# Kernel tuning notes

Measured on AMD Instinct MI355X. Metric: run time of the kernel, lower is better.

Reference implementation:

```python
import jax, jax.numpy as jnp
import numpy as np

B, C, H, W = 2, 256, 32, 32
PK, CK = 256, 256


def setup_inputs() -> dict:
    key = jax.random.key(0)
    ks = jax.random.split(key, 9)
    s = 1.0 / np.sqrt(C)
    return {
        'x': jax.random.normal(ks[0], (B, C, H, W), jnp.float32),
        'primary_indices': jax.random.randint(ks[1], (B, PK), 0, B * H * W),
        'compare_indices': jax.random.randint(ks[2], (B, CK), 0, B * H * W),
        'pre_w': jax.random.uniform(ks[3], (3, C, C), jnp.float32, -s, s),
        'pre_b': jax.random.uniform(ks[4], (3, C), jnp.float32, -s, s),
        'post_w': jax.random.uniform(ks[5], (2, C, C), jnp.float32, -s, s),
        'post_b': jax.random.uniform(ks[6], (2, C), jnp.float32, -s, s),
        'post_out_w': jax.random.uniform(ks[7], (2, C), jnp.float32, -s, s),
        'post_out_b': jax.random.uniform(ks[8], (2,), jnp.float32, -s, s),
    }


def reference(x, primary_indices, compare_indices, pre_w, pre_b,
              post_w, post_b, post_out_w, post_out_b):
    # pre_compare: stack of 1x1 convs (c->c->c->c), ReLU between layers
    h = x
    for i in range(3):
        h = jnp.einsum('bchw,oc->bohw', h, pre_w[i]) + pre_b[i][None, :, None, None]
        if i < 2:
            h = jax.nn.relu(h)
    bs, c, hh, ww = h.shape
    # flatten to [bs*h*w, c] node features (matches torch transpose+reshape)
    flat = h.reshape(bs, c, hh * ww).transpose(0, 2, 1).reshape(bs * hh * ww, c)
    # gather primary / compare node features with global flat indices
    xp = flat[primary_indices.reshape(-1)].reshape(bs, -1, c).transpose(0, 2, 1)  # [b,c,pk]
    xc = flat[compare_indices.reshape(-1)].reshape(bs, -1, c).transpose(0, 2, 1)  # [b,c,ck]
    # broadcast pairwise squared difference -> [b,c,pk,ck]
    xx = (xp[:, :, :, None] - xc[:, :, None, :]) ** 2
    # post_compare: 1x1 conv stack c->c->c->2, ReLU between layers
    g = xx
    for i in range(2):
        g = jax.nn.relu(jnp.einsum('bcpq,oc->bopq', g, post_w[i]) + post_b[i][None, :, None, None])
    out = jnp.einsum('bcpq,oc->bopq', g, post_out_w) + post_out_b[None, :, None, None]
    return out  # [b, 2, pk, ck]
```

## Files before the change

### kernel.cpp

```cpp
#include <hip/hip_runtime.h>

typedef unsigned short u16;
typedef short bf16x8 __attribute__((ext_vector_type(8)));
typedef float f32x4 __attribute__((ext_vector_type(4)));
typedef u16 u16x4 __attribute__((ext_vector_type(4)));

__device__ __forceinline__ float b2f(u16 h) {
  unsigned u = ((unsigned)h) << 16;
  return __builtin_bit_cast(float, u);
}
__device__ __forceinline__ u16 f2b(float f) {
  unsigned u = __builtin_bit_cast(unsigned, f);
  u = u + 0x7fffu + ((u >> 16) & 1u);
  return (u16)(u >> 16);
}
__device__ __forceinline__ void gld_lds16(const void* g, void* l) {
  __builtin_amdgcn_global_load_lds(
      (__attribute__((address_space(1))) void*)(g),
      (__attribute__((address_space(3))) void*)(l), 16, 0, 0);
}

__global__ void dense_edge_prep(const float* __restrict__ x,
                                const float* __restrict__ pre_w,
                                const float* __restrict__ post_w,
                                u16* __restrict__ wb, u16* __restrict__ xt) {
  const int blk = blockIdx.x;
  const int t = threadIdx.x;
  if (blk < 160) {
    const int id = blk * 256 + t;
    const int layer = id >> 13;
    const int sid = id & 8191;
    const int m = sid >> 5;
    const int s8 = sid & 31;
    const float* src = (layer < 2) ? (post_w + layer * 65536)
                                   : (pre_w + (layer - 2) * 65536);
    u16* dst = wb + layer * 65536;
    f32x4 a = *(const f32x4*)(src + m * 256 + s8 * 8);
    f32x4 c = *(const f32x4*)(src + m * 256 + s8 * 8 + 4);
    bf16x8 o;
#pragma unroll
    for (int j = 0; j < 4; j++) o[j] = (short)f2b(a[j]);
#pragma unroll
    for (int j = 0; j < 4; j++) o[4 + j] = (short)f2b(c[j]);
    *(bf16x8*)(dst + (s8 * 256 + m) * 8) = o;
  } else {
    __shared__ float tile[32 * 65];
    const int xb = blk - 160;
    const int b = xb >> 7;
    const int ct = (xb >> 4) & 7;
    const int ht = xb & 15;
    const int c0 = ct * 32, hw0 = ht * 64;
#pragma unroll
    for (int rep = 0; rep < 8; rep++) {
      const int idx = rep * 256 + t;
      const int cl = idx >> 6, hl = idx & 63;
      tile[cl * 65 + hl] = x[(b * 256 + c0 + cl) * 1024 + hw0 + hl];
    }
    __syncthreads();
    const int hl = t >> 2, c8 = t & 3;
    bf16x8 o;
#pragma unroll
    for (int i = 0; i < 8; i++) o[i] = (short)f2b(tile[(c8 * 8 + i) * 65 + hl]);
    *(bf16x8*)(xt + (b * 1024 + hw0 + hl) * 256 + c0 + c8 * 8) = o;
  }
}

__global__ __launch_bounds__(256, 2) void dense_edge_pre(
    const u16* __restrict__ xt, const u16* __restrict__ wpre,
    const float* __restrict__ preb, u16* __restrict__ flat) {
  __shared__ u16 feat[2][4096];
  const int t = threadIdx.x;
  const int wv = t >> 6, ln = t & 63;
  const int nb = blockIdx.x * 16;
  const int q4 = ln >> 4, r15 = ln & 15;

#pragma unroll
  for (int i = 0; i < 2; i++) {
    const int slot = wv * 128 + i * 64 + ln;
    const int s8 = slot >> 4, nl = slot & 15;
    gld_lds16(xt + (nb + nl) * 256 + s8 * 8, &feat[0][slot * 8]);
  }
  __syncthreads();

#pragma unroll
  for (int l = 0; l < 3; l++) {
    const u16* wl = wpre + l * 65536;
    f32x4 acc[4];
    f32x4 zero = {0.f, 0.f, 0.f, 0.f};
#pragma unroll
    for (int mt = 0; mt < 4; mt++) acc[mt] = zero;
#pragma unroll
    for (int s = 0; s < 8; s++) {
      bf16x8 bv = *(const bf16x8*)(&feat[l & 1][((s * 4 + q4) * 16 + r15) * 8]);
#pragma unroll
      for (int mt = 0; mt < 4; mt++) {
        bf16x8 av = *(const bf16x8*)(wl + ((s * 4 + q4) * 256 + wv * 64 + mt * 16 + r15) * 8);
        acc[mt] = __builtin_amdgcn_mfma_f32_16x16x32_bf16(av, bv, acc[mt], 0, 0, 0);
      }
    }
    if (l < 2) {
#pragma unroll
      for (int mt = 0; mt < 4; mt++) {
        const int o = wv * 64 + mt * 16 + q4 * 4;
        f32x4 bb = *(const f32x4*)(preb + l * 256 + o);
        u16x4 pk;
#pragma unroll
        for (int r = 0; r < 4; r++) {
          float v = fmaxf(acc[mt][r] + bb[r], 0.f);
          pk[r] = f2b(v);
        }
        *(u16x4*)(&feat[(l + 1) & 1][((o >> 3) * 16 + r15) * 8 + (o & 7)]) = pk;
      }
      __syncthreads();
    } else {
#pragma unroll
      for (int mt = 0; mt < 4; mt++) {
        const int o = wv * 64 + mt * 16 + q4 * 4;
        f32x4 bb = *(const f32x4*)(preb + 512 + o);
        u16x4 pk;
#pragma unroll
        for (int r = 0; r < 4; r++) pk[r] = f2b(acc[mt][r] + bb[r]);
        *(u16x4*)(flat + (nb + r15) * 256 + o) = pk;
      }
    }
  }
}

__global__ __launch_bounds__(512, 2) void dense_edge_main(
    const u16* __restrict__ flat, const int* __restrict__ pidx,
    const int* __restrict__ cidx, const u16* __restrict__ w1s,
    const u16* __restrict__ w2s, const float* __restrict__ b1,
    const float* __restrict__ b2, const float* __restrict__ w3,
    const float* __restrict__ b3, float* __restrict__ out) {
  __shared__ u16 xxbuf[16384];
  __shared__ u16 t1buf[16384];
  __shared__ float pbuf[4][2][64];

  const int t = threadIdx.x;
  const int wv = t >> 6;
  const int ln = t & 63;
  const int q4 = ln >> 4, r15 = ln & 15;
  const bool prod = wv < 4;
  const int cw = wv & 3;
  const int blk = blockIdx.x;
  const int tile0 = blk * 8;
  const int b = tile0 >> 10;
  const int pt = (tile0 >> 5) & 31;
  const int qt0 = tile0 & 31;
  const int p0 = pt * 8;

  const u16* wsrc = prod ? w1s : w2s;
  bf16x8 af_w[4][8];
#pragma unroll
  for (int s = 0; s < 8; s++)
#pragma unroll
    for (int mt = 0; mt < 4; mt++)
      af_w[mt][s] = *(const bf16x8*)(wsrc + ((s * 4 + q4) * 256 + cw * 64 + mt * 16 + r15) * 8);

  int pn = 0;
  if (prod) pn = pidx[b * 256 + p0 + (ln >> 3)];
  const u16* prow = flat + pn * 256 + cw * 64;

#pragma unroll 1
  for (int j = 0; j <= 8; j++) {
    if (prod) {
      if (j < 8) {
        const int qn = cidx[b * 256 + (qt0 + j) * 8 + (ln & 7)];
        const u16* qrow = flat + qn * 256 + cw * 64;
#pragma unroll
        for (int i = 0; i < 8; i++) {
          bf16x8 av = *(const bf16x8*)(prow + i * 8);
          bf16x8 bv = *(const bf16x8*)(qrow + i * 8);
          bf16x8 ov;
#pragma unroll
          for (int jj = 0; jj < 8; jj++) {
            float d = b2f((u16)av[jj]) - b2f((u16)bv[jj]);
            ov[jj] = (short)f2b(d * d);
          }
          *(bf16x8*)(xxbuf + ((cw * 8 + i) * 64 + ln) * 8) = ov;
        }
      }
    } else if (j > 0) {
      f32x4 acc[4][4];
      {
        f32x4 zero = {0.f, 0.f, 0.f, 0.f};
#pragma unroll
        for (int mt = 0; mt < 4; mt++)
#pragma unroll
          for (int nt = 0; nt < 4; nt++) acc[mt][nt] = zero;
      }
#pragma unroll
      for (int s = 0; s < 8; s++) {
        bf16x8 bfr[4];
#pragma unroll
        for (int nt = 0; nt < 4; nt++)
          bfr[nt] = *(const bf16x8*)(t1buf + ((s * 4 + q4) * 64 + nt * 16 + r15) * 8);
#pragma unroll
        for (int mt = 0; mt < 4; mt++)
#pragma unroll
          for (int nt = 0; nt < 4; nt++)
            acc[mt][nt] = __builtin_amdgcn_mfma_f32_16x16x32_bf16(af_w[mt][s], bfr[nt], acc[mt][nt], 0, 0, 0);
      }
      float part[2][4] = {{0.f, 0.f, 0.f, 0.f}, {0.f, 0.f, 0.f, 0.f}};
#pragma unroll
      for (int mt = 0; mt < 4; mt++) {
        const int o = cw * 64 + mt * 16 + q4 * 4;
        f32x4 bb = *(const f32x4*)(b2 + o);
        f32x4 w3a = *(const f32x4*)(w3 + o);
        f32x4 w3b = *(const f32x4*)(w3 + 256 + o);
#pragma unroll
        for (int nt = 0; nt < 4; nt++) {
#pragma unroll
          for (int r = 0; r < 4; r++) {
            float v = fmaxf(acc[mt][nt][r] + bb[r], 0.f);
            part[0][nt] += v * w3a[r];
            part[1][nt] += v * w3b[r];
          }
        }
      }
#pragma unroll
      for (int o3 = 0; o3 < 2; o3++)
#pragma unroll
        for (int nt = 0; nt < 4; nt++) {
          part[o3][nt] += __shfl_xor(part[o3][nt], 16, 64);
          part[o3][nt] += __shfl_xor(part[o3][nt], 32, 64);
        }
      if (q4 == 0) {
#pragma unroll
        for (int o3 = 0; o3 < 2; o3++)
#pragma unroll
          for (int nt = 0; nt < 4; nt++)
            pbuf[cw][o3][nt * 16 + r15] = part[o3][nt];
      }
    }
    __syncthreads();

    if (prod) {
      if (j < 8) {
        f32x4 acc[4][4];
        {
          f32x4 zero = {0.f, 0.f, 0.f, 0.f};
#pragma unroll
          for (int mt = 0; mt < 4; mt++)
#pragma unroll
            for (int nt = 0; nt < 4; nt++) acc[mt][nt] = zero;
        }
#pragma unroll
        for (int s = 0; s < 8; s++) {
          bf16x8 bfr[4];
#pragma unroll
          for (int nt = 0; nt < 4; nt++)
            bfr[nt] = *(const bf16x8*)(xxbuf + ((s * 4 + q4) * 64 + nt * 16 + r15) * 8);
#pragma unroll
          for (int mt = 0; mt < 4; mt++)
#pragma unroll
            for (int nt = 0; nt < 4; nt++)
              acc[mt][nt] = __builtin_amdgcn_mfma_f32_16x16x32_bf16(af_w[mt][s], bfr[nt], acc[mt][nt], 0, 0, 0);
        }
#pragma unroll
        for (int mt = 0; mt < 4; mt++) {
          const int o = cw * 64 + mt * 16 + q4 * 4;
          f32x4 bb = *(const f32x4*)(b1 + o);
#pragma unroll
          for (int nt = 0; nt < 4; nt++) {
            const int nn = nt * 16 + r15;
            u16x4 pk;
#pragma unroll
            for (int r = 0; r < 4; r++) {
              float v = fmaxf(acc[mt][nt][r] + bb[r], 0.f);
              pk[r] = f2b(v);
            }
            *(u16x4*)(t1buf + ((o >> 3) * 64 + nn) * 8 + (o & 7)) = pk;
          }
        }
      }
    } else if (j > 0) {
      const int idx = t & 255;
      if (idx < 128) {
        const int o3 = idx >> 6;
        const int n = idx & 63;
        float v = pbuf[0][o3][n] + pbuf[1][o3][n] + pbuf[2][o3][n] + pbuf[3][o3][n] + b3[o3];
        out[((b * 2 + o3) * 256 + p0 + (n >> 3)) * 256 + (qt0 + j - 1) * 8 + (n & 7)] = v;
      }
    }
    __syncthreads();
  }
}

extern "C" void kernel_launch(void* const* d_in, const int* in_sizes, int n_in,
                              void* d_out, int out_size, void* d_ws, size_t ws_size,
                              hipStream_t stream) {
  (void)in_sizes; (void)n_in; (void)out_size; (void)ws_size;
  const float* x          = (const float*)d_in[0];
  const int*   pidx       = (const int*)d_in[1];
  const int*   cidx       = (const int*)d_in[2];
  const float* pre_w      = (const float*)d_in[3];
  const float* pre_b      = (const float*)d_in[4];
  const float* post_w     = (const float*)d_in[5];
  const float* post_b     = (const float*)d_in[6];
  const float* post_out_w = (const float*)d_in[7];
  const float* post_out_b = (const float*)d_in[8];
  float* out = (float*)d_out;

  u16* ws   = (u16*)d_ws;
  u16* wb   = ws;
  u16* w1s  = wb;
  u16* w2s  = wb + 65536;
  u16* wpre = wb + 131072;
  u16* xt   = ws + 327680;
  u16* flat = ws + 851968;

  dense_edge_prep<<<416, 256, 0, stream>>>(x, pre_w, post_w, wb, xt);
  dense_edge_pre<<<128, 256, 0, stream>>>(xt, wpre, pre_b, flat);
  dense_edge_main<<<256, 512, 0, stream>>>(flat, pidx, cidx, w1s, w2s,
                                           post_b, post_b + 256,
                                           post_out_w, post_out_b, out);
}
```

Baseline: 124.3 us.

## Fuse prep into pre-conv kernel, double main-kernel waves, use packed bf16 converts

Merges the weight/input prep kernel and the pre-compare conv kernel into one launch. The pre-conv weights are now read as fp32 from global memory and converted in-register rather than pre-converted, and the x transpose is done through LDS inside the conv kernel. The main kernel goes from 512 to 1024 threads, with 8 producer and 8 consumer waves each covering 32 output channels instead of 64, which lowers per-wave register use. bf16 rounding uses the packed hardware convert when it is available. This removes one launch and the xt round trip, at the cost of redundant fp32 weight loads and converts in every pre-conv block.

```diff
diff --git a/kernel.cpp b/kernel.cpp
--- a/kernel.cpp
+++ b/kernel.cpp
@@ -14,77 +14,91 @@
   u = u + 0x7fffu + ((u >> 16) & 1u);
   return (u16)(u >> 16);
 }
-__device__ __forceinline__ void gld_lds16(const void* g, void* l) {
-  __builtin_amdgcn_global_load_lds(
-      (__attribute__((address_space(1))) void*)(g),
-      (__attribute__((address_space(3))) void*)(l), 16, 0, 0);
-}
-
-__global__ void dense_edge_prep(const float* __restrict__ x,
-                                const float* __restrict__ pre_w,
-                                const float* __restrict__ post_w,
-                                u16* __restrict__ wb, u16* __restrict__ xt) {
+
+#if defined(__has_builtin)
+#if __has_builtin(__builtin_amdgcn_cvt_pk_bf16_f32)
+#define HAVE_CVT_PK_BF16 1
+#endif
+#endif
+
+__device__ __forceinline__ unsigned f2b_pk(float a, float b) {
+#ifdef HAVE_CVT_PK_BF16
+  auto v = __builtin_amdgcn_cvt_pk_bf16_f32(a, b);
+  unsigned r;
+  __builtin_memcpy(&r, &v, 4);
+  return r;
+#else
+  return (unsigned)f2b(a) | (((unsigned)f2b(b)) << 16);
+#endif
+}
+__device__ __forceinline__ bf16x8 pack8(const float* v) {
+  union { unsigned u[4]; bf16x8 o; } r;
+  r.u[0] = f2b_pk(v[0], v[1]);
+  r.u[1] = f2b_pk(v[2], v[3]);
+  r.u[2] = f2b_pk(v[4], v[5]);
+  r.u[3] = f2b_pk(v[6], v[7]);
+  return r.o;
+}
+__device__ __forceinline__ u16x4 pack4(float a, float b, float c, float d) {
+  union { unsigned u[2]; u16x4 o; } r;
+  r.u[0] = f2b_pk(a, b);
+  r.u[1] = f2b_pk(c, d);
+  return r.o;
+}
+
+__global__ __launch_bounds__(256, 2) void dense_edge_k1(
+    const float* __restrict__ x, const float* __restrict__ pre_w,
+    const float* __restrict__ preb, const float* __restrict__ post_w,
+    u16* __restrict__ wpost, u16* __restrict__ flat) {
   const int blk = blockIdx.x;
   const int t = threadIdx.x;
-  if (blk < 160) {
-    const int id = blk * 256 + t;
+  if (blk >= 128) {
+    const int id = (blk - 128) * 256 + t;
     const int layer = id >> 13;
     const int sid = id & 8191;
     const int m = sid >> 5;
     const int s8 = sid & 31;
-    const float* src = (layer < 2) ? (post_w + layer * 65536)
-                                   : (pre_w + (layer - 2) * 65536);
-    u16* dst = wb + layer * 65536;
-    f32x4 a = *(const f32x4*)(src + m * 256 + s8 * 8);
-    f32x4 c = *(const f32x4*)(src + m * 256 + s8 * 8 + 4);
-    bf16x8 o;
-#pragma unroll
-    for (int j = 0; j < 4; j++) o[j] = (short)f2b(a[j]);
-#pragma unroll
-    for (int j = 0; j < 4; j++) o[4 + j] = (short)f2b(c[j]);
-    *(bf16x8*)(dst + (s8 * 256 + m) * 8) = o;
-  } else {
-    __shared__ float tile[32 * 65];
-    const int xb = blk - 160;
-    const int b = xb >> 7;
-    const int ct = (xb >> 4) & 7;
-    const int ht = xb & 15;
-    const int c0 = ct * 32, hw0 = ht * 64;
-#pragma unroll
-    for (int rep = 0; rep < 8; rep++) {
-      const int idx = rep * 256 + t;
-      const int cl = idx >> 6, hl = idx & 63;
-      tile[cl * 65 + hl] = x[(b * 256 + c0 + cl) * 1024 + hw0 + hl];
-    }
-    __syncthreads();
-    const int hl = t >> 2, c8 = t & 3;
-    bf16x8 o;
-#pragma unroll
-    for (int i = 0; i < 8; i++) o[i] = (short)f2b(tile[(c8 * 8 + i) * 65 + hl]);
-    *(bf16x8*)(xt + (b * 1024 + hw0 + hl) * 256 + c0 + c8 * 8) = o;
-  }
-}
-
-__global__ __launch_bounds__(256, 2) void dense_edge_pre(
-    const u16* __restrict__ xt, const u16* __restrict__ wpre,
-    const float* __restrict__ preb, u16* __restrict__ flat) {
+    const float* src = post_w + layer * 65536 + m * 256 + s8 * 8;
+    f32x4 a = *(const f32x4*)(src);
+    f32x4 c = *(const f32x4*)(src + 4);
+    float tmp[8] = {a[0], a[1], a[2], a[3], c[0], c[1], c[2], c[3]};
+    *(bf16x8*)(wpost + layer * 65536 + (s8 * 256 + m) * 8) = pack8(tmp);
+    return;
+  }
+  __shared__ float xtile[256 * 20];
   __shared__ u16 feat[2][4096];
-  const int t = threadIdx.x;
   const int wv = t >> 6, ln = t & 63;
-  const int nb = blockIdx.x * 16;
   const int q4 = ln >> 4, r15 = ln & 15;
-
-#pragma unroll
-  for (int i = 0; i < 2; i++) {
-    const int slot = wv * 128 + i * 64 + ln;
-    const int s8 = slot >> 4, nl = slot & 15;
-    gld_lds16(xt + (nb + nl) * 256 + s8 * 8, &feat[0][slot * 8]);
+  const int nb = blk * 16;
+  const int b = nb >> 10;
+  const int hw0 = nb & 1023;
+
+  {
+    const float* src = x + (b * 256 + t) * 1024 + hw0;
+    f32x4 v0 = *(const f32x4*)(src);
+    f32x4 v1 = *(const f32x4*)(src + 4);
+    f32x4 v2 = *(const f32x4*)(src + 8);
+    f32x4 v3 = *(const f32x4*)(src + 12);
+    *(f32x4*)&xtile[t * 20 + 0] = v0;
+    *(f32x4*)&xtile[t * 20 + 4] = v1;
+    *(f32x4*)&xtile[t * 20 + 8] = v2;
+    *(f32x4*)&xtile[t * 20 + 12] = v3;
   }
   __syncthreads();
+#pragma unroll
+  for (int rep = 0; rep < 2; rep++) {
+    const int id = rep * 256 + t;
+    const int n = id & 15, s8 = id >> 4;
+    float tmp[8];
+#pragma unroll
+    for (int j = 0; j < 8; j++) tmp[j] = xtile[(s8 * 8 + j) * 20 + n];
+    *(bf16x8*)(&feat[0][(s8 * 16 + n) * 8]) = pack8(tmp);
+  }
+  __syncthreads();
 
 #pragma unroll
   for (int l = 0; l < 3; l++) {
-    const u16* wl = wpre + l * 65536;
+    const float* wl = pre_w + l * 65536;
     f32x4 acc[4];
     f32x4 zero = {0.f, 0.f, 0.f, 0.f};
 #pragma unroll
@@ -94,7 +108,11 @@
       bf16x8 bv = *(const bf16x8*)(&feat[l & 1][((s * 4 + q4) * 16 + r15) * 8]);
 #pragma unroll
       for (int mt = 0; mt < 4; mt++) {
-        bf16x8 av = *(const bf16x8*)(wl + ((s * 4 + q4) * 256 + wv * 64 + mt * 16 + r15) * 8);
+        const float* wp = wl + (wv * 64 + mt * 16 + r15) * 256 + (s * 4 + q4) * 8;
+        f32x4 wa = *(const f32x4*)(wp);
+        f32x4 wc = *(const f32x4*)(wp + 4);
+        float tmp[8] = {wa[0], wa[1], wa[2], wa[3], wc[0], wc[1], wc[2], wc[3]};
+        bf16x8 av = pack8(tmp);
         acc[mt] = __builtin_amdgcn_mfma_f32_16x16x32_bf16(av, bv, acc[mt], 0, 0, 0);
       }
     }
@@ -103,13 +121,12 @@
       for (int mt = 0; mt < 4; mt++) {
         const int o = wv * 64 + mt * 16 + q4 * 4;
         f32x4 bb = *(const f32x4*)(preb + l * 256 + o);
-        u16x4 pk;
-#pragma unroll
-        for (int r = 0; r < 4; r++) {
-          float v = fmaxf(acc[mt][r] + bb[r], 0.f);
-          pk[r] = f2b(v);
-        }
-        *(u16x4*)(&feat[(l + 1) & 1][((o >> 3) * 16 + r15) * 8 + (o & 7)]) = pk;
+        float v0 = fmaxf(acc[mt][0] + bb[0], 0.f);
+        float v1 = fmaxf(acc[mt][1] + bb[1], 0.f);
+        float v2 = fmaxf(acc[mt][2] + bb[2], 0.f);
+        float v3 = fmaxf(acc[mt][3] + bb[3], 0.f);
+        *(u16x4*)(&feat[(l + 1) & 1][((o >> 3) * 16 + r15) * 8 + (o & 7)]) =
+            pack4(v0, v1, v2, v3);
       }
       __syncthreads();
     } else {
@@ -117,16 +134,15 @@
       for (int mt = 0; mt < 4; mt++) {
         const int o = wv * 64 + mt * 16 + q4 * 4;
         f32x4 bb = *(const f32x4*)(preb + 512 + o);
-        u16x4 pk;
-#pragma unroll
-        for (int r = 0; r < 4; r++) pk[r] = f2b(acc[mt][r] + bb[r]);
-        *(u16x4*)(flat + (nb + r15) * 256 + o) = pk;
+        *(u16x4*)(flat + (nb + r15) * 256 + o) =
+            pack4(acc[mt][0] + bb[0], acc[mt][1] + bb[1],
+                  acc[mt][2] + bb[2], acc[mt][3] + bb[3]);
       }
     }
   }
 }
 
-__global__ __launch_bounds__(512, 2) void dense_edge_main(
+__global__ __launch_bounds__(1024, 4) void dense_edge_main(
     const u16* __restrict__ flat, const int* __restrict__ pidx,
     const int* __restrict__ cidx, const u16* __restrict__ w1s,
     const u16* __restrict__ w2s, const float* __restrict__ b1,
@@ -134,14 +150,14 @@
     const float* __restrict__ b3, float* __restrict__ out) {
   __shared__ u16 xxbuf[16384];
   __shared__ u16 t1buf[16384];
-  __shared__ float pbuf[4][2][64];
+  __shared__ float pbuf[8][2][64];
 
   const int t = threadIdx.x;
   const int wv = t >> 6;
   const int ln = t & 63;
   const int q4 = ln >> 4, r15 = ln & 15;
-  const bool prod = wv < 4;
-  const int cw = wv & 3;
+  const bool prod = wv < 8;
+  const int cw = wv & 7;
   const int blk = blockIdx.x;
   const int tile0 = blk * 8;
   const int b = tile0 >> 10;
@@ -150,42 +166,42 @@
   const int p0 = pt * 8;
 
   const u16* wsrc = prod ? w1s : w2s;
-  bf16x8 af_w[4][8];
+  bf16x8 af_w[2][8];
 #pragma unroll
   for (int s = 0; s < 8; s++)
 #pragma unroll
-    for (int mt = 0; mt < 4; mt++)
-      af_w[mt][s] = *(const bf16x8*)(wsrc + ((s * 4 + q4) * 256 + cw * 64 + mt * 16 + r15) * 8);
+    for (int mt = 0; mt < 2; mt++)
+      af_w[mt][s] = *(const bf16x8*)(wsrc + ((s * 4 + q4) * 256 + cw * 32 + mt * 16 + r15) * 8);
 
   int pn = 0;
   if (prod) pn = pidx[b * 256 + p0 + (ln >> 3)];
-  const u16* prow = flat + pn * 256 + cw * 64;
+  const u16* prow = flat + pn * 256 + cw * 32;
 
 #pragma unroll 1
   for (int j = 0; j <= 8; j++) {
     if (prod) {
       if (j < 8) {
         const int qn = cidx[b * 256 + (qt0 + j) * 8 + (ln & 7)];
-        const u16* qrow = flat + qn * 256 + cw * 64;
-#pragma unroll
-        for (int i = 0; i < 8; i++) {
+        const u16* qrow = flat + qn * 256 + cw * 32;
+#pragma unroll
+        for (int i = 0; i < 4; i++) {
           bf16x8 av = *(const bf16x8*)(prow + i * 8);
           bf16x8 bv = *(const bf16x8*)(qrow + i * 8);
-          bf16x8 ov;
+          float d[8];
 #pragma unroll
           for (int jj = 0; jj < 8; jj++) {
-            float d = b2f((u16)av[jj]) - b2f((u16)bv[jj]);
-            ov[jj] = (short)f2b(d * d);
+            float dv = b2f((u16)av[jj]) - b2f((u16)bv[jj]);
+            d[jj] = dv * dv;
           }
-          *(bf16x8*)(xxbuf + ((cw * 8 + i) * 64 + ln) * 8) = ov;
+          *(bf16x8*)(xxbuf + ((cw * 4 + i) * 64 + ln) * 8) = pack8(d);
         }
       }
     } else if (j > 0) {
-      f32x4 acc[4][4];
+      f32x4 acc[2][4];
       {
         f32x4 zero = {0.f, 0.f, 0.f, 0.f};
 #pragma unroll
-        for (int mt = 0; mt < 4; mt++)
+        for (int mt = 0; mt < 2; mt++)
 #pragma unroll
           for (int nt = 0; nt < 4; nt++) acc[mt][nt] = zero;
       }
@@ -196,15 +212,15 @@
         for (int nt = 0; nt < 4; nt++)
           bfr[nt] = *(const bf16x8*)(t1buf + ((s * 4 + q4) * 64 + nt * 16 + r15) * 8);
 #pragma unroll
-        for (int mt = 0; mt < 4; mt++)
+        for (int mt = 0; mt < 2; mt++)
 #pragma unroll
           for (int nt = 0; nt < 4; nt++)
             acc[mt][nt] = __builtin_amdgcn_mfma_f32_16x16x32_bf16(af_w[mt][s], bfr[nt], acc[mt][nt], 0, 0, 0);
       }
       float part[2][4] = {{0.f, 0.f, 0.f, 0.f}, {0.f, 0.f, 0.f, 0.f}};
 #pragma unroll
-      for (int mt = 0; mt < 4; mt++) {
-        const int o = cw * 64 + mt * 16 + q4 * 4;
+      for (int mt = 0; mt < 2; mt++) {
+        const int o = cw * 32 + mt * 16 + q4 * 4;
         f32x4 bb = *(const f32x4*)(b2 + o);
         f32x4 w3a = *(const f32x4*)(w3 + o);
         f32x4 w3b = *(const f32x4*)(w3 + 256 + o);
@@ -237,11 +253,11 @@
 
     if (prod) {
       if (j < 8) {
-        f32x4 acc[4][4];
+        f32x4 acc[2][4];
         {
           f32x4 zero = {0.f, 0.f, 0.f, 0.f};
 #pragma unroll
-          for (int mt = 0; mt < 4; mt++)
+          for (int mt = 0; mt < 2; mt++)
 #pragma unroll
             for (int nt = 0; nt < 4; nt++) acc[mt][nt] = zero;
         }
@@ -252,34 +268,35 @@
           for (int nt = 0; nt < 4; nt++)
             bfr[nt] = *(const bf16x8*)(xxbuf + ((s * 4 + q4) * 64 + nt * 16 + r15) * 8);
 #pragma unroll
-          for (int mt = 0; mt < 4; mt++)
+          for (int mt = 0; mt < 2; mt++)
 #pragma unroll
             for (int nt = 0; nt < 4; nt++)
               acc[mt][nt] = __builtin_amdgcn_mfma_f32_16x16x32_bf16(af_w[mt][s], bfr[nt], acc[mt][nt], 0, 0, 0);
         }
 #pragma unroll
-        for (int mt = 0; mt < 4; mt++) {
-          const int o = cw * 64 + mt * 16 + q4 * 4;
+        for (int mt = 0; mt < 2; mt++) {
+          const int o = cw * 32 + mt * 16 + q4 * 4;
           f32x4 bb = *(const f32x4*)(b1 + o);
 #pragma unroll
           for (int nt = 0; nt < 4; nt++) {
             const int nn = nt * 16 + r15;
-            u16x4 pk;
-#pragma unroll
-            for (int r = 0; r < 4; r++) {
-              float v = fmaxf(acc[mt][nt][r] + bb[r], 0.f);
-              pk[r] = f2b(v);
-            }
-            *(u16x4*)(t1buf + ((o >> 3) * 64 + nn) * 8 + (o & 7)) = pk;
+            float v0 = fmaxf(acc[mt][nt][0] + bb[0], 0.f);
+            float v1 = fmaxf(acc[mt][nt][1] + bb[1], 0.f);
+            float v2 = fmaxf(acc[mt][nt][2] + bb[2], 0.f);
+            float v3 = fmaxf(acc[mt][nt][3] + bb[3], 0.f);
+            *(u16x4*)(t1buf + ((o >> 3) * 64 + nn) * 8 + (o & 7)) =
+                pack4(v0, v1, v2, v3);
           }
         }
       }
     } else if (j > 0) {
-      const int idx = t & 255;
+      const int idx = cw * 64 + ln;
       if (idx < 128) {
         const int o3 = idx >> 6;
         const int n = idx & 63;
-        float v = pbuf[0][o3][n] + pbuf[1][o3][n] + pbuf[2][o3][n] + pbuf[3][o3][n] + b3[o3];
+        float v = b3[o3];
+#pragma unroll
+        for (int w = 0; w < 8; w++) v += pbuf[w][o3][n];
         out[((b * 2 + o3) * 256 + p0 + (n >> 3)) * 256 + (qt0 + j - 1) * 8 + (n & 7)] = v;
       }
     }
@@ -303,16 +320,12 @@
   float* out = (float*)d_out;
 
   u16* ws   = (u16*)d_ws;
-  u16* wb   = ws;
-  u16* w1s  = wb;
-  u16* w2s  = wb + 65536;
-  u16* wpre = wb + 131072;
-  u16* xt   = ws + 327680;
-  u16* flat = ws + 851968;
-
-  dense_edge_prep<<<416, 256, 0, stream>>>(x, pre_w, post_w, wb, xt);
-  dense_edge_pre<<<128, 256, 0, stream>>>(xt, wpre, pre_b, flat);
-  dense_edge_main<<<256, 512, 0, stream>>>(flat, pidx, cidx, w1s, w2s,
-                                           post_b, post_b + 256,
-                                           post_out_w, post_out_b, out);
-}
+  u16* w1s  = ws;
+  u16* w2s  = ws + 65536;
+  u16* flat = ws + 131072;
+
+  dense_edge_k1<<<192, 256, 0, stream>>>(x, pre_w, pre_b, post_w, w1s, flat);
+  dense_edge_main<<<256, 1024, 0, stream>>>(flat, pidx, cidx, w1s, w2s,
+                                            post_b, post_b + 256,
+                                            post_out_w, post_out_b, out);
+}
```

After: 142.5 us. +14.7%, slower.
